# Kernel optimization log

Hardware: AMD Instinct MI355X
Metric: run time of the kernel (lower is better)

## Reference

```python
import jax, jax.numpy as jnp
import numpy as np

LN_EPS = 1e-5

def _ln(x, g):
    # LayerNorm with no bias, matching torch (population variance)
    m = x.mean(-1, keepdims=True)
    v = x.var(-1, keepdims=True)
    return (x - m) / jnp.sqrt(v + LN_EPS) * g


def setup_inputs() -> dict:
    key = jax.random.key(0)
    ks = jax.random.split(key, 10)
    B, S, D, L, V = 4, 4096, 256, 6, 32000
    std = 0.02  # nn.init.normal_(std=0.02)
    tokens = jax.random.randint(ks[0], (B, S), 0, V)
    wte = jax.random.normal(ks[1], (V, D), jnp.float32) * std
    wpe = jax.random.normal(ks[2], (S + 1, D), jnp.float32) * std  # context_size+1 table
    g_e = jnp.ones((D,), jnp.float32)
    g_p = jnp.ones((D,), jnp.float32)
    g_out = jnp.ones((D,), jnp.float32)
    ff_w1 = jax.random.normal(ks[3], (D, 4 * D), jnp.float32) * std
    ff_w2 = jax.random.normal(ks[4], (4 * D, D), jnp.float32) * std
    Wq = jax.random.normal(ks[5], (L, D, D), jnp.float32) * std
    Wk = jax.random.normal(ks[6], (L, D, D), jnp.float32) * std
    Wv = jax.random.normal(ks[7], (L, D, D), jnp.float32) * std
    return {"tokens": tokens, "wte": wte, "wpe": wpe, "g_e": g_e, "g_p": g_p,
            "g_out": g_out, "ff_w1": ff_w1, "ff_w2": ff_w2,
            "Wq": Wq, "Wk": Wk, "Wv": Wv}


def reference(tokens, wte, wpe, g_e, g_p, g_out, ff_w1, ff_w2, Wq, Wk, Wv):
    B, S = tokens.shape
    D = wte.shape[1]
    L = Wq.shape[0]
    # embeddings + pre-LN (dropout = identity at eval)
    e = _ln(wte[tokens], g_e)                 # [B,S,D] token stream
    p = _ln(wpe[:S], g_p)                     # [S,D]   positional stream (batch-invariant)
    x = e + p[None]                           # [B,S,D]
    # covariate FF on positional stream (use_ppe=True): p = p + W2 @ gelu(W1 @ p)
    p = p + jax.nn.gelu(p @ ff_w1, approximate=False) @ ff_w2
    causal = jnp.tril(jnp.ones((S, S), bool))
    inv_sqrt_d = D ** -0.5
    for l in range(L):
        # use_ppe: Q=K from positional stream (batch-invariant), V from token embeds
        q = p @ Wq[l]                          # [S,D]
        k = p @ Wk[l]                          # [S,D]
        v = jnp.einsum('bsd,de->bse', e, Wv[l])  # [B,S,D]
        s = (q @ k.T) * inv_sqrt_d             # [S,S], shared across batch
        s = jnp.where(causal, s, -jnp.inf)
        a = jax.nn.softmax(s, axis=-1)
        x = x + jnp.einsum('st,btd->bsd', a, v)
    # targets=None path: last position only
    x = x[:, -1:, :]                           # [B,1,D]
    x = _ln(x, g_out)                          # use_ln_out
    logits = x @ _ln(wte, g_e).T               # tied output head through ln_e
    return logits                              # [B,1,V]
```

## Files before the change

kernel.cpp:

```cpp
#include <hip/hip_runtime.h>
#include <hip/hip_bf16.h>

#define LN_EPS 1e-5f

typedef __attribute__((ext_vector_type(8))) short s8v;
typedef __attribute__((ext_vector_type(4))) float f32x4;

__device__ __forceinline__ float wred_sum(float v) {
#pragma unroll
  for (int o = 32; o > 0; o >>= 1) v += __shfl_xor(v, o, 64);
  return v;
}
__device__ __forceinline__ float wred_max(float v) {
#pragma unroll
  for (int o = 32; o > 0; o >>= 1) v = fmaxf(v, __shfl_xor(v, o, 64));
  return v;
}
__device__ __forceinline__ float bsum256(float v, float* s4) {
  v = wred_sum(v);
  int lane = threadIdx.x & 63, w = threadIdx.x >> 6;
  __syncthreads();
  if (lane == 0) s4[w] = v;
  __syncthreads();
  return s4[0] + s4[1] + s4[2] + s4[3];
}
__device__ __forceinline__ float bf2f(unsigned short u) {
  union { unsigned int i; float f; } c;
  c.i = ((unsigned int)u) << 16;
  return c.f;
}
__device__ __forceinline__ unsigned short f2bf(float f) {
  __hip_bfloat16 h = (__hip_bfloat16)f;
  return *(unsigned short*)&h;
}
__device__ __forceinline__ void async_cp16(const __hip_bfloat16* g, __hip_bfloat16* l) {
  __builtin_amdgcn_global_load_lds(
      (const __attribute__((address_space(1))) unsigned int*)g,
      (__attribute__((address_space(3))) unsigned int*)l, 16, 0, 0);
}

__global__ void prep_k(const float* __restrict__ wpe, const float* __restrict__ wte,
                       const int* __restrict__ tokens,
                       const float* __restrict__ g_p, const float* __restrict__ g_e,
                       const float* __restrict__ ff_w1, const float* __restrict__ ff_w2,
                       float* __restrict__ p0, unsigned short* __restrict__ p0b,
                       unsigned short* __restrict__ e,
                       unsigned short* __restrict__ w1T, unsigned short* __restrict__ w2T,
                       float* __restrict__ zeros) {
  __shared__ float lds[64][65];
  int bx = blockIdx.x, t = threadIdx.x;
  int w = t >> 6, lane = t & 63;

  if (bx < 5120) {
    int row;
    const float* g;
    const float4* src;
    if (bx < 1024) {
      row = bx * 4 + w;
      src = (const float4*)(wpe + (size_t)row * 256);
      g = g_p;
    } else {
      row = (bx - 1024) * 4 + w;
      int tok = tokens[row];
      src = (const float4*)(wte + (size_t)tok * 256);
      g = g_e;
    }
    float4 v = src[lane];
    float mean = wred_sum(v.x + v.y + v.z + v.w) * (1.f / 256.f);
    float4 d = {v.x - mean, v.y - mean, v.z - mean, v.w - mean};
    float var = wred_sum(d.x * d.x + d.y * d.y + d.z * d.z + d.w * d.w) * (1.f / 256.f);
    float r = rsqrtf(var + LN_EPS);
    float4 gv = ((const float4*)g)[lane];
    float4 o = {d.x * r * gv.x, d.y * r * gv.y, d.z * r * gv.z, d.w * r * gv.w};
    ushort4 ob = {f2bf(o.x), f2bf(o.y), f2bf(o.z), f2bf(o.w)};
    if (bx < 1024) {
      ((float4*)(p0 + (size_t)row * 256))[lane] = o;
      ((ushort4*)(p0b + (size_t)row * 256))[lane] = ob;
    } else {
      ((ushort4*)(e + (size_t)row * 256))[lane] = ob;
    }
    return;
  }
  if (bx < 5248) {
    const float* in; unsigned short* out; int M, N, bxx, byy;
    if (bx < 5184) { int i = bx - 5120; in = ff_w1; out = w1T; M = 256; N = 1024; bxx = i & 3; byy = i >> 2; }
    else           { int i = bx - 5184; in = ff_w2; out = w2T; M = 1024; N = 256; bxx = i & 15; byy = i >> 4; }
    int x = t & 63, y4 = t >> 6;
    int r0 = bxx * 64, c0 = byy * 64;
#pragma unroll
    for (int i = 0; i < 16; ++i) {
      int r = y4 * 16 + i;
      lds[r][x] = in[(size_t)(r0 + r) * N + c0 + x];
    }
    __syncthreads();
#pragma unroll
    for (int i = 0; i < 16; ++i) {
      int a = y4 * 16 + i;
      out[(size_t)(c0 + a) * M + r0 + x] = f2bf(lds[x][a]);
    }
    return;
  }
  for (int i = t; i < 6144 + 1536 + 1024; i += 256) zeros[i] = 0.f;
}

template <int TM>
__global__ __launch_bounds__(256) void mfma_gemm(
    const __hip_bfloat16* __restrict__ A, const __hip_bfloat16* __restrict__ BT,
    __hip_bfloat16* __restrict__ Cout, const float* __restrict__ res,
    int M, int N, int K, int mode) {
  constexpr int BM = TM * 32;
  __shared__ __hip_bfloat16 As[BM * 64];
  __shared__ __hip_bfloat16 Bs[64 * 64];
  const int t = threadIdx.x;
  const int lane = t & 63, wave = t >> 6;
  const int wr = wave >> 1, wc = wave & 1;
  const int fr = lane & 15, quad = lane >> 4;
  const int m0 = blockIdx.x * BM, n0 = blockIdx.y * 64;

  f32x4 acc[TM][2];
#pragma unroll
  for (int i = 0; i < TM; ++i)
#pragma unroll
    for (int j = 0; j < 2; ++j) acc[i][j] = (f32x4){0.f, 0.f, 0.f, 0.f};

  for (int k0 = 0; k0 < K; k0 += 64) {
    __syncthreads();
#pragma unroll
    for (int j = 0; j < TM; ++j) {
      int ld = wave * TM + j;
      int slot = ld * 64 + lane;
      int m = slot >> 3, c = slot & 7;
      const __hip_bfloat16* g = A + (size_t)(m0 + m) * K + k0 + ((c ^ (m & 7)) << 3);
      async_cp16(g, As + ld * 512);
    }
#pragma unroll
    for (int j = 0; j < 2; ++j) {
      int ld = wave * 2 + j;
      int slot = ld * 64 + lane;
      int n = slot >> 3, c = slot & 7;
      const __hip_bfloat16* g = BT + (size_t)(n0 + n) * K + k0 + ((c ^ (n & 7)) << 3);
      async_cp16(g, Bs + ld * 512);
    }
    __syncthreads();
#pragma unroll
    for (int h = 0; h < 2; ++h) {
      s8v af[TM], bfv[2];
#pragma unroll
      for (int i = 0; i < TM; ++i) {
        int m = wr * TM * 16 + i * 16 + fr;
        int ch = (h * 4 + quad) ^ (m & 7);
        af[i] = *(const s8v*)(As + m * 64 + ch * 8);
      }
#pragma unroll
      for (int j = 0; j < 2; ++j) {
        int n = wc * 32 + j * 16 + fr;
        int ch = (h * 4 + quad) ^ (n & 7);
        bfv[j] = *(const s8v*)(Bs + n * 64 + ch * 8);
      }
#pragma unroll
      for (int i = 0; i < TM; ++i)
#pragma unroll
        for (int j = 0; j < 2; ++j)
          acc[i][j] = __builtin_amdgcn_mfma_f32_16x16x32_bf16(af[i], bfv[j], acc[i][j], 0, 0, 0);
    }
  }

#pragma unroll
  for (int i = 0; i < TM; ++i) {
#pragma unroll
    for (int j = 0; j < 2; ++j) {
#pragma unroll
      for (int r = 0; r < 4; ++r) {
        int row = m0 + wr * TM * 16 + i * 16 + quad * 4 + r;
        int col = n0 + wc * 32 + j * 16 + fr;
        float v = acc[i][j][r];
        if (mode == 1) v = 0.5f * v * (1.f + erff(v * 0.70710678118654752f));
        if (mode == 2) v += res[(size_t)row * N + col];
        Cout[(size_t)row * N + col] = (__hip_bfloat16)v;
      }
    }
  }
}

__global__ void q_k(const __hip_bfloat16* __restrict__ pB, const float* __restrict__ Wq,
                    float* __restrict__ qall) {
  int c = blockIdx.x, l = blockIdx.y, t = threadIdx.x;
  const __hip_bfloat16* plast = pB + (size_t)4095 * 256;
  const float* W = Wq + (size_t)l * 65536;
  float pa = 0.f;
#pragma unroll
  for (int i = 0; i < 16; ++i) {
    int d = c * 16 + i;
    pa += (float)plast[d] * W[d * 256 + t];
  }
  atomicAdd(&qall[l * 256 + t], pa);
}

__global__ void kv_k(const float* __restrict__ Wk, const float* __restrict__ qall,
                     float* __restrict__ kv) {
  int l = blockIdx.y;
  int w = threadIdx.x >> 6, lane = threadIdx.x & 63;
  int r = blockIdx.x * 4 + w;
  float4 wv = ((const float4*)(Wk + (size_t)l * 65536 + (size_t)r * 256))[lane];
  float4 qv = ((const float4*)(qall + l * 256))[lane];
  float dot = wred_sum(wv.x * qv.x + wv.y * qv.y + wv.z * qv.z + wv.w * qv.w);
  if (lane == 0) kv[l * 256 + r] = dot;
}

__global__ void scores_k(const __hip_bfloat16* __restrict__ pB, const float* __restrict__ kv,
                         float* __restrict__ sc) {
  int w = threadIdx.x >> 6, lane = threadIdx.x & 63;
  int t = blockIdx.x * 4 + w;
  ushort4 pv = ((const ushort4*)((const unsigned short*)pB + (size_t)t * 256))[lane];
  float4 p = {bf2f(pv.x), bf2f(pv.y), bf2f(pv.z), bf2f(pv.w)};
#pragma unroll
  for (int l = 0; l < 6; ++l) {
    float4 kvv = ((const float4*)(kv + l * 256))[lane];
    float dot = p.x * kvv.x + p.y * kvv.y + p.z * kvv.z + p.w * kvv.w;
    dot = wred_sum(dot);
    if (lane == 0) sc[(size_t)l * 4096 + t] = dot * 0.0625f;
  }
}

__global__ void softmax_k(const float* __restrict__ sc, float* __restrict__ w) {
  int l = blockIdx.x, t = threadIdx.x;
  float4 v = ((const float4*)(sc + (size_t)l * 4096))[t];
  float m = fmaxf(fmaxf(v.x, v.y), fmaxf(v.z, v.w));
  m = wred_max(m);
  __shared__ float red[16];
  __shared__ float red2[16];
  int lane = t & 63, wv = t >> 6;
  if (lane == 0) red[wv] = m;
  __syncthreads();
  float mm = red[0];
#pragma unroll
  for (int i = 1; i < 16; ++i) mm = fmaxf(mm, red[i]);
  float e0 = expf(v.x - mm), e1 = expf(v.y - mm), e2 = expf(v.z - mm), e3 = expf(v.w - mm);
  float s = wred_sum(e0 + e1 + e2 + e3);
  if (lane == 0) red2[wv] = s;
  __syncthreads();
  float tot = 0.f;
#pragma unroll
  for (int i = 0; i < 16; ++i) tot += red2[i];
  float inv = 1.f / tot;
  float4 o = {e0 * inv, e1 * inv, e2 * inv, e3 * inv};
  ((float4*)(w + (size_t)l * 4096))[t] = o;
}

__global__ void ctx_k(const unsigned short* __restrict__ e, const float* __restrict__ w,
                      float* __restrict__ ctx) {
  int c = blockIdx.x, b = blockIdx.y, t = threadIdx.x;
  const unsigned short* eb = e + ((size_t)b * 4096 + c * 64) * 256;
  const float* w0 = w + c * 64;
  float a[6] = {0.f, 0.f, 0.f, 0.f, 0.f, 0.f};
#pragma unroll 4
  for (int i = 0; i < 64; ++i) {
    float ev = bf2f(eb[(size_t)i * 256 + t]);
#pragma unroll
    for (int l = 0; l < 6; ++l) a[l] += w0[l * 4096 + i] * ev;
  }
#pragma unroll
  for (int l = 0; l < 6; ++l) atomicAdd(&ctx[(l * 4 + b) * 256 + t], a[l]);
}

__global__ void proj_k(const float* __restrict__ ctx, const float* __restrict__ Wv,
                       float* __restrict__ xacc) {
  int c = blockIdx.x, l = blockIdx.y, t = threadIdx.x;
  const float* W = Wv + (size_t)l * 65536;
  float pa[4] = {0.f, 0.f, 0.f, 0.f};
#pragma unroll
  for (int i = 0; i < 16; ++i) {
    int d = c * 16 + i;
    float wv = W[d * 256 + t];
#pragma unroll
    for (int b = 0; b < 4; ++b) pa[b] += ctx[(l * 4 + b) * 256 + d] * wv;
  }
#pragma unroll
  for (int b = 0; b < 4; ++b) atomicAdd(&xacc[b * 256 + t], pa[b]);
}

__global__ void final_k(const unsigned short* __restrict__ e, const float* __restrict__ p0,
                        const float* __restrict__ xacc, const float* __restrict__ gout,
                        float* __restrict__ xln) {
  int b = blockIdx.x, t = threadIdx.x;
  float v = xacc[b * 256 + t] + bf2f(e[((size_t)(b * 4096 + 4095)) * 256 + t]) +
            p0[(size_t)4095 * 256 + t];
  __shared__ float s4[4];
  float mean = bsum256(v, s4) * (1.f / 256.f);
  float d = v - mean;
  float var = bsum256(d * d, s4) * (1.f / 256.f);
  xln[b * 256 + t] = d * rsqrtf(var + LN_EPS) * gout[t];
}

__global__ void logits_k(const float* __restrict__ wte, const float* __restrict__ ge,
                         const float* __restrict__ xln, float* __restrict__ out) {
  int wv = threadIdx.x >> 6, lane = threadIdx.x & 63;
  int v = blockIdx.x * 4 + wv;
  float4 x = ((const float4*)(wte + (size_t)v * 256))[lane];
  float mean = wred_sum(x.x + x.y + x.z + x.w) * (1.f / 256.f);
  float4 d = {x.x - mean, x.y - mean, x.z - mean, x.w - mean};
  float var = wred_sum(d.x * d.x + d.y * d.y + d.z * d.z + d.w * d.w) * (1.f / 256.f);
  float r = rsqrtf(var + LN_EPS);
  float4 gv = ((const float4*)ge)[lane];
  float4 ln = {d.x * r * gv.x, d.y * r * gv.y, d.z * r * gv.z, d.w * r * gv.w};
#pragma unroll
  for (int b = 0; b < 4; ++b) {
    float4 xv = ((const float4*)(xln + b * 256))[lane];
    float dot = wred_sum(ln.x * xv.x + ln.y * xv.y + ln.z * xv.z + ln.w * xv.w);
    if (lane == 0) out[b * 32000 + v] = dot;
  }
}

#define O_P0    ((size_t)0)
#define O_E     ((size_t)1048576)
#define O_P0B   ((size_t)3145728)
#define O_W1T   ((size_t)3670016)
#define O_W2T   ((size_t)3801088)
#define O_HB    ((size_t)3932160)
#define O_PB    ((size_t)6029312)
#define O_CTX   ((size_t)6553600)
#define O_QALL  ((size_t)6559744)
#define O_XACC  ((size_t)6561280)
#define O_KV    ((size_t)6562304)
#define O_SC    ((size_t)6563840)
#define O_WSM   ((size_t)6588416)
#define O_XLN   ((size_t)6612992)

extern "C" void kernel_launch(void* const* d_in, const int* in_sizes, int n_in,
                              void* d_out, int out_size, void* d_ws, size_t ws_size,
                              hipStream_t stream) {
  const int*   tokens = (const int*)d_in[0];
  const float* wte    = (const float*)d_in[1];
  const float* wpe    = (const float*)d_in[2];
  const float* g_e    = (const float*)d_in[3];
  const float* g_p    = (const float*)d_in[4];
  const float* g_out  = (const float*)d_in[5];
  const float* ff_w1  = (const float*)d_in[6];
  const float* ff_w2  = (const float*)d_in[7];
  const float* Wq     = (const float*)d_in[8];
  const float* Wk     = (const float*)d_in[9];
  const float* Wv     = (const float*)d_in[10];
  float* out = (float*)d_out;
  float* ws = (float*)d_ws;

  float* p0 = ws + O_P0;
  unsigned short* e   = (unsigned short*)(ws + O_E);
  unsigned short* p0b = (unsigned short*)(ws + O_P0B);
  unsigned short* w1T = (unsigned short*)(ws + O_W1T);
  unsigned short* w2T = (unsigned short*)(ws + O_W2T);
  __hip_bfloat16* hB  = (__hip_bfloat16*)(ws + O_HB);
  __hip_bfloat16* pB  = (__hip_bfloat16*)(ws + O_PB);
  float* ctx  = ws + O_CTX;
  float* qall = ws + O_QALL;
  float* xacc = ws + O_XACC;
  float* kv   = ws + O_KV;
  float* sc   = ws + O_SC;
  float* wsm  = ws + O_WSM;
  float* xln  = ws + O_XLN;

  prep_k<<<5249, 256, 0, stream>>>(wpe, wte, tokens, g_p, g_e, ff_w1, ff_w2,
                                   p0, p0b, e, w1T, w2T, ctx);
  mfma_gemm<4><<<dim3(32, 16), 256, 0, stream>>>(
      (const __hip_bfloat16*)p0b, (const __hip_bfloat16*)w1T, hB, nullptr, 4096, 1024, 256, 1);
  mfma_gemm<2><<<dim3(64, 4), 256, 0, stream>>>(
      hB, (const __hip_bfloat16*)w2T, pB, p0, 4096, 256, 1024, 2);
  q_k<<<dim3(16, 6), 256, 0, stream>>>(pB, Wq, qall);
  kv_k<<<dim3(64, 6), 256, 0, stream>>>(Wk, qall, kv);
  scores_k<<<1024, 256, 0, stream>>>(pB, kv, sc);
  softmax_k<<<6, 1024, 0, stream>>>(sc, wsm);
  ctx_k<<<dim3(64, 4), 256, 0, stream>>>(e, wsm, ctx);
  proj_k<<<dim3(16, 6), 256, 0, stream>>>(ctx, Wv, xacc);
  final_k<<<4, 256, 0, stream>>>(e, p0, xacc, g_out, xln);
  logits_k<<<8000, 256, 0, stream>>>(wte, g_e, xln, out);
}
```

Measured before the change: 165.7 us.

## Eliminate second FF GEMM by folding W2 into key-query vectors algebraically

The second feed-forward GEMM that built the full positional stream is gone. The last positional row is computed directly (plast_k), and scores are formed as p0·kv + h·(W2·kv), using a precomputed W2·kv per layer, in a fused sc_k kernel that reads h and p0 once. This avoids writing and re-reading the 4096x256 p stream and the W2 transpose, and drops the fp32 p0 buffer. The first GEMM tile and ctx_k grid also change. In exchange, scores are now computed from bf16 h with fp32 weights, which changes rounding slightly.

Result: slower. 198.4 us (+19.7%).

```diff
diff --git a/kernel.cpp b/kernel.cpp
--- a/kernel.cpp
+++ b/kernel.cpp
@@ -42,11 +42,9 @@
 __global__ void prep_k(const float* __restrict__ wpe, const float* __restrict__ wte,
                        const int* __restrict__ tokens,
                        const float* __restrict__ g_p, const float* __restrict__ g_e,
-                       const float* __restrict__ ff_w1, const float* __restrict__ ff_w2,
-                       float* __restrict__ p0, unsigned short* __restrict__ p0b,
-                       unsigned short* __restrict__ e,
-                       unsigned short* __restrict__ w1T, unsigned short* __restrict__ w2T,
-                       float* __restrict__ zeros) {
+                       const float* __restrict__ ff_w1,
+                       unsigned short* __restrict__ p0b, unsigned short* __restrict__ e,
+                       unsigned short* __restrict__ w1T, float* __restrict__ zeros) {
   __shared__ float lds[64][65];
   int bx = blockIdx.x, t = threadIdx.x;
   int w = t >> 6, lane = t & 63;
@@ -71,43 +69,37 @@
     float var = wred_sum(d.x * d.x + d.y * d.y + d.z * d.z + d.w * d.w) * (1.f / 256.f);
     float r = rsqrtf(var + LN_EPS);
     float4 gv = ((const float4*)g)[lane];
-    float4 o = {d.x * r * gv.x, d.y * r * gv.y, d.z * r * gv.z, d.w * r * gv.w};
-    ushort4 ob = {f2bf(o.x), f2bf(o.y), f2bf(o.z), f2bf(o.w)};
-    if (bx < 1024) {
-      ((float4*)(p0 + (size_t)row * 256))[lane] = o;
-      ((ushort4*)(p0b + (size_t)row * 256))[lane] = ob;
-    } else {
-      ((ushort4*)(e + (size_t)row * 256))[lane] = ob;
-    }
+    ushort4 ob = {f2bf(d.x * r * gv.x), f2bf(d.y * r * gv.y),
+                  f2bf(d.z * r * gv.z), f2bf(d.w * r * gv.w)};
+    if (bx < 1024) ((ushort4*)(p0b + (size_t)row * 256))[lane] = ob;
+    else           ((ushort4*)(e   + (size_t)row * 256))[lane] = ob;
     return;
   }
-  if (bx < 5248) {
-    const float* in; unsigned short* out; int M, N, bxx, byy;
-    if (bx < 5184) { int i = bx - 5120; in = ff_w1; out = w1T; M = 256; N = 1024; bxx = i & 3; byy = i >> 2; }
-    else           { int i = bx - 5184; in = ff_w2; out = w2T; M = 1024; N = 256; bxx = i & 15; byy = i >> 4; }
+  if (bx < 5184) {
+    int i = bx - 5120;
+    int bxx = i & 3, byy = i >> 2;
     int x = t & 63, y4 = t >> 6;
     int r0 = bxx * 64, c0 = byy * 64;
 #pragma unroll
-    for (int i = 0; i < 16; ++i) {
-      int r = y4 * 16 + i;
-      lds[r][x] = in[(size_t)(r0 + r) * N + c0 + x];
+    for (int k = 0; k < 16; ++k) {
+      int r = y4 * 16 + k;
+      lds[r][x] = ff_w1[(size_t)(r0 + r) * 1024 + c0 + x];
     }
     __syncthreads();
 #pragma unroll
-    for (int i = 0; i < 16; ++i) {
-      int a = y4 * 16 + i;
-      out[(size_t)(c0 + a) * M + r0 + x] = f2bf(lds[x][a]);
+    for (int k = 0; k < 16; ++k) {
+      int a = y4 * 16 + k;
+      w1T[(size_t)(c0 + a) * 256 + r0 + x] = f2bf(lds[x][a]);
     }
     return;
   }
-  for (int i = t; i < 6144 + 1536 + 1024; i += 256) zeros[i] = 0.f;
+  for (int i = t; i < 8960; i += 256) zeros[i] = 0.f;
 }
 
 template <int TM>
-__global__ __launch_bounds__(256) void mfma_gemm(
+__global__ __launch_bounds__(256, 4) void mfma_gemm(
     const __hip_bfloat16* __restrict__ A, const __hip_bfloat16* __restrict__ BT,
-    __hip_bfloat16* __restrict__ Cout, const float* __restrict__ res,
-    int M, int N, int K, int mode) {
+    __hip_bfloat16* __restrict__ Cout, int M, int N, int K, int mode) {
   constexpr int BM = TM * 32;
   __shared__ __hip_bfloat16 As[BM * 64];
   __shared__ __hip_bfloat16 Bs[64 * 64];
@@ -175,23 +167,34 @@
         int col = n0 + wc * 32 + j * 16 + fr;
         float v = acc[i][j][r];
         if (mode == 1) v = 0.5f * v * (1.f + erff(v * 0.70710678118654752f));
-        if (mode == 2) v += res[(size_t)row * N + col];
         Cout[(size_t)row * N + col] = (__hip_bfloat16)v;
       }
     }
   }
 }
 
-__global__ void q_k(const __hip_bfloat16* __restrict__ pB, const float* __restrict__ Wq,
+__global__ void plast_k(const unsigned short* __restrict__ hB,
+                        const unsigned short* __restrict__ p0b,
+                        const float* __restrict__ W2, float* __restrict__ plast) {
+  int c = blockIdx.x, t = threadIdx.x;
+  float pa = (c == 0) ? bf2f(p0b[(size_t)4095 * 256 + t]) : 0.f;
+#pragma unroll
+  for (int i = 0; i < 16; ++i) {
+    int k = c * 16 + i;
+    pa += bf2f(hB[(size_t)4095 * 1024 + k]) * W2[(size_t)k * 256 + t];
+  }
+  atomicAdd(&plast[t], pa);
+}
+
+__global__ void q_k(const float* __restrict__ plast, const float* __restrict__ Wq,
                     float* __restrict__ qall) {
   int c = blockIdx.x, l = blockIdx.y, t = threadIdx.x;
-  const __hip_bfloat16* plast = pB + (size_t)4095 * 256;
   const float* W = Wq + (size_t)l * 65536;
   float pa = 0.f;
 #pragma unroll
   for (int i = 0; i < 16; ++i) {
     int d = c * 16 + i;
-    pa += (float)plast[d] * W[d * 256 + t];
+    pa += plast[d] * W[d * 256 + t];
   }
   atomicAdd(&qall[l * 256 + t], pa);
 }
@@ -207,19 +210,61 @@
   if (lane == 0) kv[l * 256 + r] = dot;
 }
 
-__global__ void scores_k(const __hip_bfloat16* __restrict__ pB, const float* __restrict__ kv,
-                         float* __restrict__ sc) {
+__global__ void w2kv_k(const float* __restrict__ W2, const float* __restrict__ kv,
+                       float* __restrict__ w2kv) {
+  int l = blockIdx.y;
   int w = threadIdx.x >> 6, lane = threadIdx.x & 63;
-  int t = blockIdx.x * 4 + w;
-  ushort4 pv = ((const ushort4*)((const unsigned short*)pB + (size_t)t * 256))[lane];
-  float4 p = {bf2f(pv.x), bf2f(pv.y), bf2f(pv.z), bf2f(pv.w)};
+  int r = blockIdx.x * 4 + w;
+  float4 wv = ((const float4*)(W2 + (size_t)r * 256))[lane];
+  float4 qv = ((const float4*)(kv + l * 256))[lane];
+  float dot = wred_sum(wv.x * qv.x + wv.y * qv.y + wv.z * qv.z + wv.w * qv.w);
+  if (lane == 0) w2kv[l * 1024 + r] = dot;
+}
+
+__global__ void sc_k(const unsigned short* __restrict__ p0b, const unsigned short* __restrict__ hB,
+                     const float* __restrict__ kv, const float* __restrict__ w2kv,
+                     float* __restrict__ sc) {
+  __shared__ float skv[6 * 256];
+  __shared__ float sw2[6 * 1024];
+  int t = threadIdx.x;
+  for (int i = t; i < 1536; i += 256) skv[i] = kv[i];
+  for (int i = t; i < 6144; i += 256) sw2[i] = w2kv[i];
+  __syncthreads();
+  int wave = t >> 6, lane = t & 63;
+  int row0 = blockIdx.x * 16 + wave * 4;
+  ushort4 hv[4][4], pv[4];
+#pragma unroll
+  for (int rr = 0; rr < 4; ++rr) {
+    const ushort4* hrow = (const ushort4*)(hB + (size_t)(row0 + rr) * 1024);
+#pragma unroll
+    for (int c = 0; c < 4; ++c) hv[rr][c] = hrow[c * 64 + lane];
+    pv[rr] = ((const ushort4*)(p0b + (size_t)(row0 + rr) * 256))[lane];
+  }
+  float acc[6][4];
 #pragma unroll
   for (int l = 0; l < 6; ++l) {
-    float4 kvv = ((const float4*)(kv + l * 256))[lane];
-    float dot = p.x * kvv.x + p.y * kvv.y + p.z * kvv.z + p.w * kvv.w;
-    dot = wred_sum(dot);
-    if (lane == 0) sc[(size_t)l * 4096 + t] = dot * 0.0625f;
-  }
+    float4 kf = ((const float4*)(skv + l * 256))[lane];
+    float4 wf[4];
+#pragma unroll
+    for (int c = 0; c < 4; ++c) wf[c] = ((const float4*)(sw2 + l * 1024 + c * 256))[lane];
+#pragma unroll
+    for (int rr = 0; rr < 4; ++rr) {
+      float a = bf2f(pv[rr].x) * kf.x + bf2f(pv[rr].y) * kf.y +
+                bf2f(pv[rr].z) * kf.z + bf2f(pv[rr].w) * kf.w;
+#pragma unroll
+      for (int c = 0; c < 4; ++c)
+        a += bf2f(hv[rr][c].x) * wf[c].x + bf2f(hv[rr][c].y) * wf[c].y +
+             bf2f(hv[rr][c].z) * wf[c].z + bf2f(hv[rr][c].w) * wf[c].w;
+      acc[l][rr] = a;
+    }
+  }
+#pragma unroll
+  for (int l = 0; l < 6; ++l)
+#pragma unroll
+    for (int rr = 0; rr < 4; ++rr) {
+      float d = wred_sum(acc[l][rr]);
+      if (lane == 0) sc[(size_t)l * 4096 + row0 + rr] = d * 0.0625f;
+    }
 }
 
 __global__ void softmax_k(const float* __restrict__ sc, float* __restrict__ w) {
@@ -250,11 +295,11 @@
 __global__ void ctx_k(const unsigned short* __restrict__ e, const float* __restrict__ w,
                       float* __restrict__ ctx) {
   int c = blockIdx.x, b = blockIdx.y, t = threadIdx.x;
-  const unsigned short* eb = e + ((size_t)b * 4096 + c * 64) * 256;
-  const float* w0 = w + c * 64;
+  const unsigned short* eb = e + ((size_t)b * 4096 + c * 32) * 256;
+  const float* w0 = w + c * 32;
   float a[6] = {0.f, 0.f, 0.f, 0.f, 0.f, 0.f};
 #pragma unroll 4
-  for (int i = 0; i < 64; ++i) {
+  for (int i = 0; i < 32; ++i) {
     float ev = bf2f(eb[(size_t)i * 256 + t]);
 #pragma unroll
     for (int l = 0; l < 6; ++l) a[l] += w0[l * 4096 + i] * ev;
@@ -279,12 +324,12 @@
   for (int b = 0; b < 4; ++b) atomicAdd(&xacc[b * 256 + t], pa[b]);
 }
 
-__global__ void final_k(const unsigned short* __restrict__ e, const float* __restrict__ p0,
+__global__ void final_k(const unsigned short* __restrict__ e, const unsigned short* __restrict__ p0b,
                         const float* __restrict__ xacc, const float* __restrict__ gout,
                         float* __restrict__ xln) {
   int b = blockIdx.x, t = threadIdx.x;
   float v = xacc[b * 256 + t] + bf2f(e[((size_t)(b * 4096 + 4095)) * 256 + t]) +
-            p0[(size_t)4095 * 256 + t];
+            bf2f(p0b[(size_t)4095 * 256 + t]);
   __shared__ float s4[4];
   float mean = bsum256(v, s4) * (1.f / 256.f);
   float d = v - mean;
@@ -311,20 +356,19 @@
   }
 }
 
-#define O_P0    ((size_t)0)
-#define O_E     ((size_t)1048576)
-#define O_P0B   ((size_t)3145728)
-#define O_W1T   ((size_t)3670016)
-#define O_W2T   ((size_t)3801088)
-#define O_HB    ((size_t)3932160)
-#define O_PB    ((size_t)6029312)
-#define O_CTX   ((size_t)6553600)
-#define O_QALL  ((size_t)6559744)
-#define O_XACC  ((size_t)6561280)
-#define O_KV    ((size_t)6562304)
-#define O_SC    ((size_t)6563840)
-#define O_WSM   ((size_t)6588416)
-#define O_XLN   ((size_t)6612992)
+#define O_E     ((size_t)0)
+#define O_P0B   ((size_t)2097152)
+#define O_W1T   ((size_t)2621440)
+#define O_HB    ((size_t)2752512)
+#define O_CTX   ((size_t)4849664)
+#define O_QALL  ((size_t)4855808)
+#define O_XACC  ((size_t)4857344)
+#define O_PLAST ((size_t)4858368)
+#define O_KV    ((size_t)4858624)
+#define O_W2KV  ((size_t)4860160)
+#define O_SC    ((size_t)4866304)
+#define O_WSM   ((size_t)4890880)
+#define O_XLN   ((size_t)4915456)
 
 extern "C" void kernel_launch(void* const* d_in, const int* in_sizes, int n_in,
                               void* d_out, int out_size, void* d_ws, size_t ws_size,
@@ -343,33 +387,33 @@
   float* out = (float*)d_out;
   float* ws = (float*)d_ws;
 
-  float* p0 = ws + O_P0;
   unsigned short* e   = (unsigned short*)(ws + O_E);
   unsigned short* p0b = (unsigned short*)(ws + O_P0B);
   unsigned short* w1T = (unsigned short*)(ws + O_W1T);
-  unsigned short* w2T = (unsigned short*)(ws + O_W2T);
-  __hip_bfloat16* hB  = (__hip_bfloat16*)(ws + O_HB);
-  __hip_bfloat16* pB  = (__hip_bfloat16*)(ws + O_PB);
-  float* ctx  = ws + O_CTX;
-  float* qall = ws + O_QALL;
-  float* xacc = ws + O_XACC;
-  float* kv   = ws + O_KV;
-  float* sc   = ws + O_SC;
-  float* wsm  = ws + O_WSM;
-  float* xln  = ws + O_XLN;
-
-  prep_k<<<5249, 256, 0, stream>>>(wpe, wte, tokens, g_p, g_e, ff_w1, ff_w2,
-                                   p0, p0b, e, w1T, w2T, ctx);
-  mfma_gemm<4><<<dim3(32, 16), 256, 0, stream>>>(
-      (const __hip_bfloat16*)p0b, (const __hip_bfloat16*)w1T, hB, nullptr, 4096, 1024, 256, 1);
-  mfma_gemm<2><<<dim3(64, 4), 256, 0, stream>>>(
-      hB, (const __hip_bfloat16*)w2T, pB, p0, 4096, 256, 1024, 2);
-  q_k<<<dim3(16, 6), 256, 0, stream>>>(pB, Wq, qall);
+  unsigned short* hB  = (unsigned short*)(ws + O_HB);
+  float* ctx   = ws + O_CTX;
+  float* qall  = ws + O_QALL;
+  float* xacc  = ws + O_XACC;
+  float* plast = ws + O_PLAST;
+  float* kv    = ws + O_KV;
+  float* w2kv  = ws + O_W2KV;
+  float* sc    = ws + O_SC;
+  float* wsm   = ws + O_WSM;
+  float* xln   = ws + O_XLN;
+
+  prep_k<<<5185, 256, 0, stream>>>(wpe, wte, tokens, g_p, g_e, ff_w1,
+                                   p0b, e, w1T, ctx);
+  mfma_gemm<2><<<dim3(64, 16), 256, 0, stream>>>(
+      (const __hip_bfloat16*)p0b, (const __hip_bfloat16*)w1T,
+      (__hip_bfloat16*)hB, 4096, 1024, 256, 1);
+  plast_k<<<64, 256, 0, stream>>>(hB, p0b, ff_w2, plast);
+  q_k<<<dim3(16, 6), 256, 0, stream>>>(plast, Wq, qall);
   kv_k<<<dim3(64, 6), 256, 0, stream>>>(Wk, qall, kv);
-  scores_k<<<1024, 256, 0, stream>>>(pB, kv, sc);
+  w2kv_k<<<dim3(256, 6), 256, 0, stream>>>(ff_w2, kv, w2kv);
+  sc_k<<<256, 256, 0, stream>>>(p0b, hB, kv, w2kv, sc);
   softmax_k<<<6, 1024, 0, stream>>>(sc, wsm);
-  ctx_k<<<dim3(64, 4), 256, 0, stream>>>(e, wsm, ctx);
+  ctx_k<<<dim3(128, 4), 256, 0, stream>>>(e, wsm, ctx);
   proj_k<<<dim3(16, 6), 256, 0, stream>>>(ctx, Wv, xacc);
-  final_k<<<4, 256, 0, stream>>>(e, p0, xacc, g_out, xln);
+  final_k<<<4, 256, 0, stream>>>(e, p0b, xacc, g_out, xln);
   logits_k<<<8000, 256, 0, stream>>>(wte, g_e, xln, out);
 }
```
